# Optimization experiments

Measured on AMD Instinct MI355X. Metric: run time of the kernel, lower is better.

The kernel has to match this reference:

```python
import jax, jax.numpy as jnp
import numpy as np

B, N, D, K = 8, 2048, 256, 8192


def setup_inputs() -> dict:
    key = jax.random.key(0)
    k1, k2 = jax.random.split(key)
    x = jax.random.normal(k1, (B, N, D), dtype=jnp.float32)          # encoder output z_e (identity encoder)
    codebook = jax.random.normal(k2, (K, D), dtype=jnp.float32)      # nn.Parameter(codebook_size, codebook_dim)
    return {"x": x, "codebook": codebook}


def reference(x, codebook):
    z_e = x  # identity encoder
    # Squared Euclidean distances via matmul expansion: ||z||^2 - 2 z.c^T + ||c||^2 -> (B, N, K)
    z2 = jnp.sum(z_e * z_e, axis=-1, keepdims=True)                   # (B, N, 1)
    c2 = jnp.sum(codebook * codebook, axis=-1)                        # (K,)
    cross = jnp.einsum('bnd,kd->bnk', z_e, codebook)                  # (B, N, K)
    distances = z2 - 2.0 * cross + c2                                 # (B, N, K)
    indices = jnp.argmin(distances, axis=-1)                          # (B, N) int
    z_q = codebook[indices]                                           # gather -> (B, N, D)
    x_recon = z_q  # identity decoder
    return (x_recon, z_e, z_q, indices)
```

## Files before the change

### kernel.cpp

```cpp
#include <hip/hip_runtime.h>
#include <stdint.h>


#define M_ROWS 16384
#define D_DIM  256
#define K_CB   8192
#define NSPLIT 16
#define BM 128
#define BN 128
#define EPS 12.0f

typedef float f32x4 __attribute__((ext_vector_type(4)));
typedef int   int4v __attribute__((ext_vector_type(4)));
typedef int   int8v __attribute__((ext_vector_type(8)));

__device__ __forceinline__ void gld_lds16(const void* g, void* l) {
  __builtin_amdgcn_global_load_lds((__attribute__((address_space(1))) void*)g,
                                   (__attribute__((address_space(3))) void*)l,
                                   16, 0, 0);
}

__device__ __forceinline__ uint32_t fp8x4(const f32x4 v) {
  int p = __builtin_amdgcn_cvt_pk_fp8_f32(v[0], v[1], 0, false);
  p = __builtin_amdgcn_cvt_pk_fp8_f32(v[2], v[3], p, true);
  return (uint32_t)p;
}

__global__ __launch_bounds__(256) void prep(const float* __restrict__ x,
                                            const float* __restrict__ cb,
                                            uint8_t* __restrict__ Ap,
                                            uint8_t* __restrict__ Bp,
                                            float* __restrict__ c2) {
  const int w = threadIdx.x >> 6, lane = threadIdx.x & 63;
  if (blockIdx.x < M_ROWS / 4) {
    const int row = blockIdx.x * 4 + w;
    const f32x4 v = *(const f32x4*)(x + (size_t)row * D_DIM + lane * 4);
    *(uint32_t*)(Ap + (size_t)row * D_DIM + lane * 4) = fp8x4(v);
  } else {
    const int row = (blockIdx.x - M_ROWS / 4) * 4 + w;
    const f32x4 v = *(const f32x4*)(cb + (size_t)row * D_DIM + lane * 4);
    *(uint32_t*)(Bp + (size_t)row * D_DIM + lane * 4) = fp8x4(v);
    double s = 0.0;
#pragma unroll
    for (int t = 0; t < 4; ++t) s += (double)v[t] * (double)v[t];
#pragma unroll
    for (int m = 1; m < 64; m <<= 1) s += __shfl_xor(s, m, 64);
    if (lane == 0) c2[row] = (float)s;
  }
}

__device__ __forceinline__ int8v frag8(const uint8_t* rowp, int fq, int x7) {
  const int4v lo = *(const int4v*)(rowp + (((fq * 2)     ^ x7) << 4));
  const int4v hi = *(const int4v*)(rowp + (((fq * 2 + 1) ^ x7) << 4));
  int8v r;
#pragma unroll
  for (int t = 0; t < 4; ++t) { r[t] = lo[t]; r[4 + t] = hi[t]; }
  return r;
}

__global__ __launch_bounds__(256, 3) void vq_main(const uint8_t* __restrict__ Ap,
                                                  const uint8_t* __restrict__ Bp,
                                                  const float* __restrict__ c2,
                                                  uint2* __restrict__ part) {
  __shared__ uint8_t As[BM * 128];
  __shared__ uint8_t Bs[BN * 128];
  __shared__ uint2 sred[BM * 2];

  const int tid  = threadIdx.x;
  const int w    = tid >> 6;
  const int lane = tid & 63;
  const int wm   = w >> 1;
  const int wn   = w & 1;

  const int rowBase = blockIdx.x * BM;
  const int nBase   = blockIdx.y * (K_CB / NSPLIT);

  const int stRow  = lane >> 3;
  const int stColB = ((lane & 7) ^ stRow) * 16;

  const int fr = lane & 15;
  const int fq = lane >> 4;
  const int x7 = fr & 7;

  uint32_t t1[4][4], t2[4][4];
#pragma unroll
  for (int i = 0; i < 4; ++i)
#pragma unroll
    for (int r = 0; r < 4; ++r) { t1[i][r] = 0x7f7ffe00u; t2[i][r] = 0x7f7ffe00u; }

  for (int nit = 0; nit < (K_CB / NSPLIT) / BN; ++nit) {
    f32x4 acc[4][4];
#pragma unroll
    for (int i = 0; i < 4; ++i)
#pragma unroll
      for (int j = 0; j < 4; ++j) acc[i][j] = (f32x4){0.f, 0.f, 0.f, 0.f};

#pragma unroll
    for (int kh = 0; kh < 2; ++kh) {
      const int kb = kh * 128;
#pragma unroll
      for (int ii = 0; ii < 4; ++ii) {
        const int rt = w * 32 + ii * 8 + stRow;
        gld_lds16(Ap + (size_t)(rowBase + rt) * D_DIM + kb + stColB,
                  As + rt * 128 + (lane & 7) * 16);
      }
#pragma unroll
      for (int ii = 0; ii < 4; ++ii) {
        const int rt = w * 32 + ii * 8 + stRow;
        gld_lds16(Bp + (size_t)(nBase + nit * BN + rt) * D_DIM + kb + stColB,
                  Bs + rt * 128 + (lane & 7) * 16);
      }
      __syncthreads();
      int8v bf[4];
#pragma unroll
      for (int j = 0; j < 4; ++j)
        bf[j] = frag8(Bs + (wn * 64 + j * 16 + fr) * 128, fq, x7);
#pragma unroll
      for (int i = 0; i < 4; ++i) {
        const int8v av = frag8(As + (wm * 64 + i * 16 + fr) * 128, fq, x7);
#pragma unroll
        for (int j = 0; j < 4; ++j)
          acc[i][j] = __builtin_amdgcn_mfma_scale_f32_16x16x128_f8f6f4(
              av, bf[j], acc[i][j], 0, 0,
              0, 0x7f7f7f7f, 0, 0x7f7f7f7f);
      }
      __syncthreads();
    }

#pragma unroll
    for (int j = 0; j < 4; ++j) {
      const int col9 = nit * BN + wn * 64 + j * 16 + fr;
      const float cv = c2[nBase + col9] + 1024.0f;
#pragma unroll
      for (int i = 0; i < 4; ++i)
#pragma unroll
        for (int r = 0; r < 4; ++r) {
          const float s = fmaf(-2.0f, acc[i][j][r], cv);
          const uint32_t p = (__float_as_uint(s) & ~511u) | (uint32_t)col9;
          const uint32_t hi = t1[i][r] > p ? t1[i][r] : p;
          t1[i][r] = t1[i][r] < p ? t1[i][r] : p;
          t2[i][r] = t2[i][r] < hi ? t2[i][r] : hi;
        }
    }
  }

#pragma unroll
  for (int i = 0; i < 4; ++i)
#pragma unroll
    for (int r = 0; r < 4; ++r) {
      uint32_t a1 = t1[i][r], a2 = t2[i][r];
#pragma unroll
      for (int m = 1; m < 16; m <<= 1) {
        const uint32_t o1 = __shfl_xor(a1, m, 64);
        const uint32_t o2 = __shfl_xor(a2, m, 64);
        const uint32_t hi = a1 > o1 ? a1 : o1;
        a1 = a1 < o1 ? a1 : o1;
        const uint32_t lo2 = a2 < o2 ? a2 : o2;
        a2 = lo2 < hi ? lo2 : hi;
      }
      if (fr == 0) {
        const int row = wm * 64 + i * 16 + fq * 4 + r;
        sred[row * 2 + wn] = make_uint2(a1, a2);
      }
    }
  __syncthreads();
  if (tid < BM) {
    const uint2 a = sred[tid * 2 + 0], b = sred[tid * 2 + 1];
    const uint32_t hi = a.x > b.x ? a.x : b.x;
    const uint32_t m1 = a.x < b.x ? a.x : b.x;
    const uint32_t lo2 = a.y < b.y ? a.y : b.y;
    const uint32_t m2 = lo2 < hi ? lo2 : hi;
    part[(size_t)(rowBase + tid) * NSPLIT + blockIdx.y] = make_uint2(m1, m2);
  }
}

__global__ __launch_bounds__(256) void vq_merge(const uint2* __restrict__ part,
                                                const float* __restrict__ x,
                                                const float* __restrict__ cb,
                                                float* __restrict__ out) {
  const int w = threadIdx.x >> 6, lane = threadIdx.x & 63;
  const int row = blockIdx.x * 4 + w;

  uint32_t pk = 0x7f7ffe00u;
  int gidx = 0x7fffffff;
  if (lane < 32) {
    const uint2 pp = part[(size_t)row * NSPLIT + (lane >> 1)];
    pk = (lane & 1) ? pp.y : pp.x;
    gidx = (lane >> 1) * (K_CB / NSPLIT) + (int)(pk & 511u);
  }
  uint32_t pmin = pk;
#pragma unroll
  for (int m = 1; m < 64; m <<= 1) {
    const uint32_t o = __shfl_xor(pmin, m, 64);
    pmin = pmin < o ? pmin : o;
  }
  const float vmin = __uint_as_float(pmin & ~511u);
  const float vme  = __uint_as_float(pk & ~511u);
  const unsigned long long mask = __ballot(lane < 32 && vme <= vmin + EPS);

  const f32x4 xv = *(const f32x4*)(x + (size_t)row * D_DIM + lane * 4);

  int winner;
  if (__popcll(mask) == 1) {
    winner = __shfl(gidx, __ffsll((long long)mask) - 1, 64);
  } else {
    double bestd = 1.0e300;
    int bidx = 0x7fffffff;
    unsigned long long mm = mask;
    while (mm) {
      const int q = __ffsll((long long)mm) - 1;
      mm &= mm - 1;
      const int ci = __shfl(gidx, q, 64);
      const f32x4 cv = *(const f32x4*)(cb + (size_t)ci * D_DIM + lane * 4);
      double s = 0.0;
#pragma unroll
      for (int t = 0; t < 4; ++t) {
        const double dx = (double)xv[t] - (double)cv[t];
        s += dx * dx;
      }
#pragma unroll
      for (int m = 1; m < 64; m <<= 1) s += __shfl_xor(s, m, 64);
      if (s < bestd || (s == bestd && ci < bidx)) { bestd = s; bidx = ci; }
    }
    winner = bidx;
  }

  float* out_recon = out;
  float* out_ze    = out + (size_t)M_ROWS * D_DIM;
  float* out_zq    = out + 2 * (size_t)M_ROWS * D_DIM;
  float* out_idx   = out + 3 * (size_t)M_ROWS * D_DIM;

  const f32x4 cv = *(const f32x4*)(cb + (size_t)winner * D_DIM + lane * 4);
  *(f32x4*)(out_recon + (size_t)row * D_DIM + lane * 4) = cv;
  *(f32x4*)(out_zq    + (size_t)row * D_DIM + lane * 4) = cv;
  *(f32x4*)(out_ze    + (size_t)row * D_DIM + lane * 4) = xv;
  if (lane == 0) out_idx[row] = (float)winner;
}

extern "C" void kernel_launch(void* const* d_in, const int* in_sizes, int n_in,
                              void* d_out, int out_size, void* d_ws, size_t ws_size,
                              hipStream_t stream) {
  const float* x  = (const float*)d_in[0];
  const float* cb = (const float*)d_in[1];
  float* out = (float*)d_out;

  char* ws = (char*)d_ws;
  float*    c2   = (float*)ws;
  uint2*    part = (uint2*)(ws + 32768);
  uint8_t*  Ap   = (uint8_t*)(ws + 32768 + 2097152);
  uint8_t*  Bp   = Ap + (size_t)M_ROWS * D_DIM;
  if (ws_size < (size_t)(32768 + 2097152 + 4194304 + 2097152)) return;

  prep    <<<dim3(M_ROWS / 4 + K_CB / 4), dim3(256), 0, stream>>>(x, cb, Ap, Bp, c2);
  vq_main <<<dim3(M_ROWS / BM, NSPLIT), dim3(256), 0, stream>>>(Ap, Bp, c2, part);
  vq_merge<<<dim3(M_ROWS / 4), dim3(256), 0, stream>>>(part, x, cb, out);
}
```

Baseline: 189.7 us.

## Load MFMA fragments directly from global and keep top-4 candidates per split

Drops the LDS staging and barriers in the main FP8 MFMA loop. Each wave now reads its A and B fragments straight from global memory into registers, relying on caches for reuse. It also widens candidate tracking from top-2 to top-4 per split using a sorting network, adds round-to-3-bit-mantissa pre-rounding before the FP8 conversion, raises EPS, and lowers the occupancy hint to 2. The merge kernel now rescans more exact candidates, which costs extra register pressure, global traffic and compare work in exchange for removing synchronisation and guarding accuracy.

```diff
diff --git a/kernel.cpp b/kernel.cpp
--- a/kernel.cpp
+++ b/kernel.cpp
@@ -8,21 +8,23 @@
 #define NSPLIT 16
 #define BM 128
 #define BN 128
-#define EPS 12.0f
+#define EPS 20.0f
 
 typedef float f32x4 __attribute__((ext_vector_type(4)));
-typedef int   int4v __attribute__((ext_vector_type(4)));
 typedef int   int8v __attribute__((ext_vector_type(8)));
 
-__device__ __forceinline__ void gld_lds16(const void* g, void* l) {
-  __builtin_amdgcn_global_load_lds((__attribute__((address_space(1))) void*)g,
-                                   (__attribute__((address_space(3))) void*)l,
-                                   16, 0, 0);
+__device__ __forceinline__ uint32_t umin32(uint32_t a, uint32_t b) { return a < b ? a : b; }
+__device__ __forceinline__ uint32_t umax32(uint32_t a, uint32_t b) { return a > b ? a : b; }
+
+__device__ __forceinline__ float rtne3(float f) {
+  uint32_t u = __float_as_uint(f);
+  u = (u + 0x0007FFFFu + ((u >> 20) & 1u)) & 0xFFF00000u;
+  return __uint_as_float(u);
 }
 
 __device__ __forceinline__ uint32_t fp8x4(const f32x4 v) {
-  int p = __builtin_amdgcn_cvt_pk_fp8_f32(v[0], v[1], 0, false);
-  p = __builtin_amdgcn_cvt_pk_fp8_f32(v[2], v[3], p, true);
+  int p = __builtin_amdgcn_cvt_pk_fp8_f32(rtne3(v[0]), rtne3(v[1]), 0, false);
+  p = __builtin_amdgcn_cvt_pk_fp8_f32(rtne3(v[2]), rtne3(v[3]), p, true);
   return (uint32_t)p;
 }
 
@@ -49,22 +51,11 @@
   }
 }
 
-__device__ __forceinline__ int8v frag8(const uint8_t* rowp, int fq, int x7) {
-  const int4v lo = *(const int4v*)(rowp + (((fq * 2)     ^ x7) << 4));
-  const int4v hi = *(const int4v*)(rowp + (((fq * 2 + 1) ^ x7) << 4));
-  int8v r;
-#pragma unroll
-  for (int t = 0; t < 4; ++t) { r[t] = lo[t]; r[4 + t] = hi[t]; }
-  return r;
-}
-
-__global__ __launch_bounds__(256, 3) void vq_main(const uint8_t* __restrict__ Ap,
+__global__ __launch_bounds__(256, 2) void vq_main(const uint8_t* __restrict__ Ap,
                                                   const uint8_t* __restrict__ Bp,
                                                   const float* __restrict__ c2,
-                                                  uint2* __restrict__ part) {
-  __shared__ uint8_t As[BM * 128];
-  __shared__ uint8_t Bs[BN * 128];
-  __shared__ uint2 sred[BM * 2];
+                                                  uint4* __restrict__ part) {
+  __shared__ uint32_t sred[BM][8];
 
   const int tid  = threadIdx.x;
   const int w    = tid >> 6;
@@ -75,18 +66,20 @@
   const int rowBase = blockIdx.x * BM;
   const int nBase   = blockIdx.y * (K_CB / NSPLIT);
 
-  const int stRow  = lane >> 3;
-  const int stColB = ((lane & 7) ^ stRow) * 16;
-
   const int fr = lane & 15;
   const int fq = lane >> 4;
-  const int x7 = fr & 7;
-
-  uint32_t t1[4][4], t2[4][4];
+
+  const uint8_t* Abase = Ap + (size_t)(rowBase + wm * 64 + fr) * D_DIM + fq * 32;
+  const uint8_t* Bbase = Bp + (size_t)(nBase + wn * 64 + fr) * D_DIM + fq * 32;
+
+  uint32_t t1[4][4], t2[4][4], t3[4][4], t4[4][4];
 #pragma unroll
   for (int i = 0; i < 4; ++i)
 #pragma unroll
-    for (int r = 0; r < 4; ++r) { t1[i][r] = 0x7f7ffe00u; t2[i][r] = 0x7f7ffe00u; }
+    for (int r = 0; r < 4; ++r) {
+      t1[i][r] = 0x7f7ffe00u; t2[i][r] = 0x7f7ffe00u;
+      t3[i][r] = 0x7f7ffe00u; t4[i][r] = 0x7f7ffe00u;
+    }
 
   for (int nit = 0; nit < (K_CB / NSPLIT) / BN; ++nit) {
     f32x4 acc[4][4];
@@ -97,34 +90,20 @@
 
 #pragma unroll
     for (int kh = 0; kh < 2; ++kh) {
-      const int kb = kh * 128;
-#pragma unroll
-      for (int ii = 0; ii < 4; ++ii) {
-        const int rt = w * 32 + ii * 8 + stRow;
-        gld_lds16(Ap + (size_t)(rowBase + rt) * D_DIM + kb + stColB,
-                  As + rt * 128 + (lane & 7) * 16);
-      }
-#pragma unroll
-      for (int ii = 0; ii < 4; ++ii) {
-        const int rt = w * 32 + ii * 8 + stRow;
-        gld_lds16(Bp + (size_t)(nBase + nit * BN + rt) * D_DIM + kb + stColB,
-                  Bs + rt * 128 + (lane & 7) * 16);
-      }
-      __syncthreads();
-      int8v bf[4];
+      int8v af[4], bf[4];
+#pragma unroll
+      for (int i = 0; i < 4; ++i)
+        af[i] = *(const int8v*)(Abase + (size_t)(i * 16) * D_DIM + kh * 128);
 #pragma unroll
       for (int j = 0; j < 4; ++j)
-        bf[j] = frag8(Bs + (wn * 64 + j * 16 + fr) * 128, fq, x7);
-#pragma unroll
-      for (int i = 0; i < 4; ++i) {
-        const int8v av = frag8(As + (wm * 64 + i * 16 + fr) * 128, fq, x7);
+        bf[j] = *(const int8v*)(Bbase + (size_t)(nit * BN + j * 16) * D_DIM + kh * 128);
+#pragma unroll
+      for (int i = 0; i < 4; ++i)
 #pragma unroll
         for (int j = 0; j < 4; ++j)
           acc[i][j] = __builtin_amdgcn_mfma_scale_f32_16x16x128_f8f6f4(
-              av, bf[j], acc[i][j], 0, 0,
+              af[i], bf[j], acc[i][j], 0, 0,
               0, 0x7f7f7f7f, 0, 0x7f7f7f7f);
-      }
-      __syncthreads();
     }
 
 #pragma unroll
@@ -137,9 +116,10 @@
         for (int r = 0; r < 4; ++r) {
           const float s = fmaf(-2.0f, acc[i][j][r], cv);
           const uint32_t p = (__float_as_uint(s) & ~511u) | (uint32_t)col9;
-          const uint32_t hi = t1[i][r] > p ? t1[i][r] : p;
-          t1[i][r] = t1[i][r] < p ? t1[i][r] : p;
-          t2[i][r] = t2[i][r] < hi ? t2[i][r] : hi;
+          const uint32_t b = umax32(t1[i][r], p); t1[i][r] = umin32(t1[i][r], p);
+          const uint32_t d = umax32(t2[i][r], b); t2[i][r] = umin32(t2[i][r], b);
+          const uint32_t f = umax32(t3[i][r], d); t3[i][r] = umin32(t3[i][r], d);
+          t4[i][r] = umin32(t4[i][r], f);
         }
     }
   }
@@ -148,46 +128,53 @@
   for (int i = 0; i < 4; ++i)
 #pragma unroll
     for (int r = 0; r < 4; ++r) {
-      uint32_t a1 = t1[i][r], a2 = t2[i][r];
+      uint32_t a1 = t1[i][r], a2 = t2[i][r], a3 = t3[i][r], a4 = t4[i][r];
 #pragma unroll
       for (int m = 1; m < 16; m <<= 1) {
-        const uint32_t o1 = __shfl_xor(a1, m, 64);
-        const uint32_t o2 = __shfl_xor(a2, m, 64);
-        const uint32_t hi = a1 > o1 ? a1 : o1;
-        a1 = a1 < o1 ? a1 : o1;
-        const uint32_t lo2 = a2 < o2 ? a2 : o2;
-        a2 = lo2 < hi ? lo2 : hi;
+        const uint32_t b1 = __shfl_xor(a1, m, 64);
+        const uint32_t b2 = __shfl_xor(a2, m, 64);
+        const uint32_t b3 = __shfl_xor(a3, m, 64);
+        const uint32_t b4 = __shfl_xor(a4, m, 64);
+        uint32_t c1 = umin32(a1, b4), c2_ = umin32(a2, b3);
+        uint32_t c3 = umin32(a3, b2), c4 = umin32(a4, b1);
+        uint32_t lo, hi;
+        lo = umin32(c1, c3); hi = umax32(c1, c3); c1 = lo; c3 = hi;
+        lo = umin32(c2_, c4); hi = umax32(c2_, c4); c2_ = lo; c4 = hi;
+        lo = umin32(c1, c2_); hi = umax32(c1, c2_); c1 = lo; c2_ = hi;
+        lo = umin32(c3, c4); hi = umax32(c3, c4); c3 = lo; c4 = hi;
+        a1 = c1; a2 = c2_; a3 = c3; a4 = c4;
       }
       if (fr == 0) {
         const int row = wm * 64 + i * 16 + fq * 4 + r;
-        sred[row * 2 + wn] = make_uint2(a1, a2);
+        sred[row][wn * 4 + 0] = a1; sred[row][wn * 4 + 1] = a2;
+        sred[row][wn * 4 + 2] = a3; sred[row][wn * 4 + 3] = a4;
       }
     }
   __syncthreads();
   if (tid < BM) {
-    const uint2 a = sred[tid * 2 + 0], b = sred[tid * 2 + 1];
-    const uint32_t hi = a.x > b.x ? a.x : b.x;
-    const uint32_t m1 = a.x < b.x ? a.x : b.x;
-    const uint32_t lo2 = a.y < b.y ? a.y : b.y;
-    const uint32_t m2 = lo2 < hi ? lo2 : hi;
-    part[(size_t)(rowBase + tid) * NSPLIT + blockIdx.y] = make_uint2(m1, m2);
-  }
-}
-
-__global__ __launch_bounds__(256) void vq_merge(const uint2* __restrict__ part,
+    uint32_t a1 = sred[tid][0], a2 = sred[tid][1], a3 = sred[tid][2], a4 = sred[tid][3];
+    const uint32_t b1 = sred[tid][4], b2 = sred[tid][5], b3 = sred[tid][6], b4 = sred[tid][7];
+    uint32_t c1 = umin32(a1, b4), c2_ = umin32(a2, b3);
+    uint32_t c3 = umin32(a3, b2), c4 = umin32(a4, b1);
+    uint32_t lo, hi;
+    lo = umin32(c1, c3); hi = umax32(c1, c3); c1 = lo; c3 = hi;
+    lo = umin32(c2_, c4); hi = umax32(c2_, c4); c2_ = lo; c4 = hi;
+    lo = umin32(c1, c2_); hi = umax32(c1, c2_); c1 = lo; c2_ = hi;
+    lo = umin32(c3, c4); hi = umax32(c3, c4); c3 = lo; c4 = hi;
+    part[(size_t)(rowBase + tid) * NSPLIT + blockIdx.y] = make_uint4(c1, c2_, c3, c4);
+  }
+}
+
+__global__ __launch_bounds__(256) void vq_merge(const uint32_t* __restrict__ part,
                                                 const float* __restrict__ x,
                                                 const float* __restrict__ cb,
                                                 float* __restrict__ out) {
   const int w = threadIdx.x >> 6, lane = threadIdx.x & 63;
   const int row = blockIdx.x * 4 + w;
 
-  uint32_t pk = 0x7f7ffe00u;
-  int gidx = 0x7fffffff;
-  if (lane < 32) {
-    const uint2 pp = part[(size_t)row * NSPLIT + (lane >> 1)];
-    pk = (lane & 1) ? pp.y : pp.x;
-    gidx = (lane >> 1) * (K_CB / NSPLIT) + (int)(pk & 511u);
-  }
+  const uint32_t pk = part[(size_t)row * 64 + lane];
+  const int gidx = (lane >> 2) * (K_CB / NSPLIT) + (int)(pk & 511u);
+
   uint32_t pmin = pk;
 #pragma unroll
   for (int m = 1; m < 64; m <<= 1) {
@@ -196,7 +183,7 @@
   }
   const float vmin = __uint_as_float(pmin & ~511u);
   const float vme  = __uint_as_float(pk & ~511u);
-  const unsigned long long mask = __ballot(lane < 32 && vme <= vmin + EPS);
+  const unsigned long long mask = __ballot(vme <= vmin + EPS);
 
   const f32x4 xv = *(const f32x4*)(x + (size_t)row * D_DIM + lane * 4);
 
@@ -246,12 +233,12 @@
 
   char* ws = (char*)d_ws;
   float*    c2   = (float*)ws;
-  uint2*    part = (uint2*)(ws + 32768);
-  uint8_t*  Ap   = (uint8_t*)(ws + 32768 + 2097152);
+  uint4*    part = (uint4*)(ws + 32768);
+  uint8_t*  Ap   = (uint8_t*)(ws + 32768 + 4194304);
   uint8_t*  Bp   = Ap + (size_t)M_ROWS * D_DIM;
-  if (ws_size < (size_t)(32768 + 2097152 + 4194304 + 2097152)) return;
+  if (ws_size < (size_t)(32768 + 4194304 + 4194304 + 2097152)) return;
 
   prep    <<<dim3(M_ROWS / 4 + K_CB / 4), dim3(256), 0, stream>>>(x, cb, Ap, Bp, c2);
   vq_main <<<dim3(M_ROWS / BM, NSPLIT), dim3(256), 0, stream>>>(Ap, Bp, c2, part);
-  vq_merge<<<dim3(M_ROWS / 4), dim3(256), 0, stream>>>(part, x, cb, out);
-}
+  vq_merge<<<dim3(M_ROWS / 4), dim3(256), 0, stream>>>((const uint32_t*)part, x, cb, out);
+}
```

Measured after the change: 218.0 us. +14.9%, slower.
